# Performance work log

Hardware: AMD Instinct MI355X
Metric: run time of the kernel (lower is better)

## Reference

```python
import jax, jax.numpy as jnp
import numpy as np

D_MODEL = 768
N_HEAD = 12
D_HEAD = D_MODEL // N_HEAD
B, T = 2, 2048


def setup_inputs() -> dict:
    key = jax.random.key(0)
    k1, k2, k3 = jax.random.split(key, 3)
    x = jax.random.normal(k1, (B, T, D_MODEL), dtype=jnp.float32)
    w_attn = jax.random.normal(k2, (D_MODEL, 3 * D_MODEL), dtype=jnp.float32) * (1.0 / np.sqrt(D_MODEL))
    b_attn = jnp.zeros((3 * D_MODEL,), dtype=jnp.float32)
    w_proj = jax.random.normal(k3, (D_MODEL, D_MODEL), dtype=jnp.float32) * (1.0 / np.sqrt(D_MODEL))
    b_proj = jnp.zeros((D_MODEL,), dtype=jnp.float32)
    return {"x": x, "w_attn": w_attn, "b_attn": b_attn, "w_proj": w_proj, "b_proj": b_proj}


def reference(x, w_attn, b_attn, w_proj, b_proj):
    Bq, Tq, C = x.shape
    qkv = x @ w_attn + b_attn                                  # [B, T, 3C]
    qkv = qkv.reshape(Bq, Tq, 3, N_HEAD, D_HEAD)
    q, k, v = qkv[:, :, 0], qkv[:, :, 1], qkv[:, :, 2]         # [B, T, H, Dh]
    scale = 1.0 / np.sqrt(D_HEAD)
    att = jnp.einsum('bqhd,bkhd->bhqk', q, k) * scale          # [B, H, T, T]
    causal = jnp.tril(jnp.ones((Tq, Tq), dtype=bool))
    att = jnp.where(causal[None, None], att, -jnp.inf)
    att = jax.nn.softmax(att, axis=-1)
    y = jnp.einsum('bhqk,bkhd->bqhd', att, v).reshape(Bq, Tq, C)
    return y @ w_proj + b_proj
```

## Files before the change

kernel.cpp:

```cpp
#include <hip/hip_runtime.h>
#include <hip/hip_bf16.h>

#define D_MODEL 768
#define N_HEADS 12
#define D_HEADK 64
#define BB 2
#define TT 2048
#define M_TOK (BB*TT)
#define N_QKV (3*D_MODEL)

using f32x4  = __attribute__((ext_vector_type(4))) float;
using f32x16 = __attribute__((ext_vector_type(16))) float;
using s16x8  = __attribute__((ext_vector_type(8))) short;

__device__ __forceinline__ float fast_exp2(float x) {
    return __builtin_amdgcn_exp2f(x);
}

__device__ __forceinline__ unsigned short f2bf(float f) {
    union { float f; unsigned u; } v; v.f = f;
    unsigned r = v.u + 0x7FFFu + ((v.u >> 16) & 1u);
    return (unsigned short)(r >> 16);
}

__device__ __forceinline__ unsigned cvtpk_bf16(float lo, float hi) {
    unsigned d;
    asm("v_cvt_pk_bf16_f32 %0, %1, %2" : "=v"(d) : "v"(lo), "v"(hi));
    return d;
}

__global__ void xbf_kernel(const float* __restrict__ X, unsigned short* __restrict__ Xb) {
    int idx = (blockIdx.x * 256 + threadIdx.x) * 8;
    float4 v0 = *(const float4*)&X[idx];
    float4 v1 = *(const float4*)&X[idx + 4];
    ushort4 u0, u1;
    u0.x = f2bf(v0.x); u0.y = f2bf(v0.y); u0.z = f2bf(v0.z); u0.w = f2bf(v0.w);
    u1.x = f2bf(v1.x); u1.y = f2bf(v1.y); u1.z = f2bf(v1.z); u1.w = f2bf(v1.w);
    *(ushort4*)&Xb[idx]     = u0;
    *(ushort4*)&Xb[idx + 4] = u1;
}

__global__ void wtrans_kernel(const float* __restrict__ Wa, const float* __restrict__ Wp,
                              unsigned short* __restrict__ Wta, unsigned short* __restrict__ Wtp) {
    const float* W; unsigned short* Wt; int N;
    if (blockIdx.z == 0) { W = Wa; Wt = Wta; N = N_QKV; }
    else                 { W = Wp; Wt = Wtp; N = D_MODEL; }
    int bx = blockIdx.x * 32;
    if (bx >= N) return;
    int by = blockIdx.y * 32;
    __shared__ float tile[32][33];
    int tx = threadIdx.x & 31;
    int ty = threadIdx.x >> 5;
    #pragma unroll
    for (int i = ty; i < 32; i += 8)
        tile[i][tx] = W[(size_t)(by + i) * N + bx + tx];
    __syncthreads();
    #pragma unroll
    for (int i = ty; i < 32; i += 8)
        Wt[(size_t)(bx + i) * D_MODEL + by + tx] = f2bf(tile[tx][i]);
}

__launch_bounds__(256)
__global__ void qkv_kernel(const unsigned short* __restrict__ Xb, const unsigned short* __restrict__ Wt,
                           const float* __restrict__ bias,
                           unsigned short* __restrict__ Qw, unsigned short* __restrict__ Kw,
                           unsigned short* __restrict__ Vw) {
    __shared__ unsigned short As[128][40];
    __shared__ unsigned short Bs[128][40];
    const int m0 = blockIdx.y * 128;
    const int n0 = blockIdx.x * 128;
    const int tid = threadIdx.x;
    const int l  = tid & 63;
    const int w  = tid >> 6;
    const int wr = w >> 1, wc = w & 1;
    const int lr = l & 15, lk = (l >> 4) * 8, li = (l >> 4) * 4;

    f32x4 acc[4][4] = {};
    for (int kt = 0; kt < D_MODEL; kt += 32) {
        #pragma unroll
        for (int p = 0; p < 2; ++p) {
            int ch = tid * 2 + p;
            int r = ch >> 2;
            int c = (ch & 3) * 8;
            *(int4*)&As[r][c] = *(const int4*)&Xb[(size_t)(m0 + r) * D_MODEL + kt + c];
            *(int4*)&Bs[r][c] = *(const int4*)&Wt[(size_t)(n0 + r) * D_MODEL + kt + c];
        }
        __syncthreads();
        s16x8 a[4], bf[4];
        #pragma unroll
        for (int mi = 0; mi < 4; ++mi)
            a[mi] = *(const s16x8*)&As[wr*64 + mi*16 + lr][lk];
        #pragma unroll
        for (int ni = 0; ni < 4; ++ni)
            bf[ni] = *(const s16x8*)&Bs[wc*64 + ni*16 + lr][lk];
        #pragma unroll
        for (int mi = 0; mi < 4; ++mi)
            #pragma unroll
            for (int ni = 0; ni < 4; ++ni)
                acc[mi][ni] = __builtin_amdgcn_mfma_f32_16x16x32_bf16(a[mi], bf[ni], acc[mi][ni], 0, 0, 0);
        __syncthreads();
    }
    #pragma unroll
    for (int ni = 0; ni < 4; ++ni) {
        int ng = n0 + wc*64 + ni*16 + lr;
        int mat = ng / D_MODEL;
        int hd  = ng % D_MODEL;
        int h = hd >> 6, d = hd & 63;
        float bv = bias[ng];
        #pragma unroll
        for (int mi = 0; mi < 4; ++mi) {
            #pragma unroll
            for (int i = 0; i < 4; ++i) {
                int t  = m0 + wr*64 + mi*16 + li + i;
                int b  = t >> 11, tq = t & 2047;
                float val = acc[mi][ni][i] + bv;
                size_t off = ((size_t)(b*N_HEADS + h)*TT + tq)*64 + d;
                if (mat == 0)      Qw[off] = f2bf(val * 0.18033688f);
                else if (mat == 1) Kw[off] = f2bf(val);
                else               Vw[off] = f2bf(val);
            }
        }
    }
}

__launch_bounds__(256)
__global__ void vtrans_kernel(const unsigned short* __restrict__ Vw, unsigned short* __restrict__ Vt) {
    __shared__ unsigned short tile[64][65];
    const int bh = blockIdx.y;
    const int t0 = blockIdx.x * 64;
    const int tid = threadIdx.x;
    const int srow = tid >> 3;
    const int scol = (tid & 7) * 8;
    const unsigned short* src = Vw + (size_t)bh * TT * 64;
    unsigned short* dst = Vt + (size_t)bh * 64 * TT;
    *(int4*)&tile[srow][scol]    = *(const int4*)&src[(size_t)(t0 + srow) * 64 + scol];
    *(int4*)&tile[srow+32][scol] = *(const int4*)&src[(size_t)(t0 + srow + 32) * 64 + scol];
    __syncthreads();
    s16x8 a0, a1;
    #pragma unroll
    for (int j = 0; j < 8; ++j) {
        a0[j] = (short)tile[scol + j][srow];
        a1[j] = (short)tile[scol + j][srow + 32];
    }
    *(s16x8*)&dst[(size_t)srow * TT + t0 + scol]        = a0;
    *(s16x8*)&dst[(size_t)(srow + 32) * TT + t0 + scol] = a1;
}

__device__ __forceinline__ int swz(int r, int c) { return r*64 + (c ^ ((r & 7) << 3)); }

__launch_bounds__(256)
__global__ void attn_kernel(const unsigned short* __restrict__ Q,
                            const unsigned short* __restrict__ Kk,
                            const unsigned short* __restrict__ Vt,
                            unsigned short* __restrict__ Y) {
    __shared__ unsigned short Ks[64*64];
    __shared__ unsigned short Vs[64*64];
    const int bh = blockIdx.y;
    const int qb = gridDim.x - 1 - blockIdx.x;
    const int q0 = qb * 128;
    const int b = bh / N_HEADS, h = bh % N_HEADS;
    const int tid = threadIdx.x;
    const int l  = tid & 63;
    const int w  = tid >> 6;
    const int lq = l & 31;
    const int hi = l >> 5;
    const int srow = tid >> 3;
    const int scol = (tid & 7) * 8;
    const int qw0 = q0 + w * 32;

    const unsigned short* Qp = Q  + (size_t)bh * TT * 64;
    const unsigned short* Kp = Kk + (size_t)bh * TT * 64;
    const unsigned short* Vp = Vt + (size_t)bh * 64 * TT;

    s16x8 qsel[4];
    {
        const unsigned short* qrow = &Qp[(size_t)(qw0 + lq) * 64];
        #pragma unroll
        for (int t = 0; t < 4; ++t) {
            s16x8 qlo = *(const s16x8*)&qrow[16*t];
            s16x8 qhi = *(const s16x8*)&qrow[16*t + 8];
            qsel[t] = hi ? qhi : qlo;
        }
    }

    float mi = -1e30f, si = 0.f;
    f32x16 o0 = {}, o1 = {};

    const int niter = 2 * (qb + 1);
    int4 kp0 = *(const int4*)&Kp[(size_t)srow * 64 + scol];
    int4 kp1 = *(const int4*)&Kp[(size_t)(srow + 32) * 64 + scol];
    int4 vp0 = *(const int4*)&Vp[(size_t)srow * TT + scol];
    int4 vp1 = *(const int4*)&Vp[(size_t)(srow + 32) * TT + scol];

    for (int it = 0; it < niter; ++it) {
        const int kt = it * 64;
        __syncthreads();
        *(int4*)&Ks[swz(srow,      scol)] = kp0;
        *(int4*)&Ks[swz(srow + 32, scol)] = kp1;
        *(int4*)&Vs[swz(srow,      scol)] = vp0;
        *(int4*)&Vs[swz(srow + 32, scol)] = vp1;
        __syncthreads();
        if (it + 1 < niter) {
            const int k2 = kt + 64;
            kp0 = *(const int4*)&Kp[(size_t)(k2 + srow) * 64 + scol];
            kp1 = *(const int4*)&Kp[(size_t)(k2 + srow + 32) * 64 + scol];
            vp0 = *(const int4*)&Vp[(size_t)srow * TT + k2 + scol];
            vp1 = *(const int4*)&Vp[(size_t)(srow + 32) * TT + k2 + scol];
        }
        #pragma unroll
        for (int kti = 0; kti < 2; ++kti) {
            const int kk = kt + kti * 32;
            if (kk > qw0) continue;
            const bool diag = (kk == qw0);
            f32x16 s = {};
            #pragma unroll
            for (int t = 0; t < 4; ++t) {
                s16x8 a = *(const s16x8*)&Ks[swz(kti*32 + lq, 16*t + 8*hi)];
                s = __builtin_amdgcn_mfma_f32_32x32x16_bf16(a, qsel[t], s, 0, 0, 0);
            }
            if (diag) {
                #pragma unroll
                for (int r = 0; r < 16; ++r) {
                    const int kloc = (r & 3) + 8*(r >> 2) + 4*hi;
                    if (kloc > lq) s[r] = -1e30f;
                }
            }
            float lm = s[0];
            #pragma unroll
            for (int r = 1; r < 16; ++r) lm = fmaxf(lm, s[r]);
            if (!__all(lm <= mi + 11.5f)) {
                float pm = fmaxf(lm, __shfl_xor(lm, 32));
                float mn = fmaxf(mi, pm);
                float sf = fast_exp2(mi - mn);
                si *= sf;
                #pragma unroll
                for (int r = 0; r < 16; ++r) {
                    const int qloc = (r & 3) + 8*(r >> 2) + 4*hi;
                    float sfq = __shfl(sf, qloc);
                    o0[r] *= sfq; o1[r] *= sfq;
                }
                mi = mn;
            }
            float e[16];
            float psum = 0.f;
            #pragma unroll
            for (int r = 0; r < 16; ++r) {
                e[r] = fast_exp2(s[r] - mi);
                psum += e[r];
            }
            si += psum;
            #pragma unroll
            for (int s2 = 0; s2 < 2; ++s2) {
                unsigned c0 = cvtpk_bf16(e[8*s2 + 0], e[8*s2 + 1]);
                unsigned c1 = cvtpk_bf16(e[8*s2 + 2], e[8*s2 + 3]);
                unsigned c2 = cvtpk_bf16(e[8*s2 + 4], e[8*s2 + 5]);
                unsigned c3 = cvtpk_bf16(e[8*s2 + 6], e[8*s2 + 7]);
                asm("v_permlane32_swap_b32 %0, %1" : "+v"(c0), "+v"(c2));
                asm("v_permlane32_swap_b32 %0, %1" : "+v"(c1), "+v"(c3));
                union { unsigned u[4]; s16x8 v; } pa;
                pa.u[0] = c0; pa.u[1] = c1; pa.u[2] = c2; pa.u[3] = c3;
                const int kc = kti*32 + 16*s2 + 8*hi;
                s16x8 vb0 = *(const s16x8*)&Vs[swz(lq,      kc)];
                s16x8 vb1 = *(const s16x8*)&Vs[swz(32 + lq, kc)];
                o0 = __builtin_amdgcn_mfma_f32_32x32x16_bf16(pa.v, vb0, o0, 0, 0, 0);
                o1 = __builtin_amdgcn_mfma_f32_32x32x16_bf16(pa.v, vb1, o1, 0, 0, 0);
            }
        }
    }
    float sfull = si + __shfl_xor(si, 32);
    float invf = 1.f / sfull;
    #pragma unroll
    for (int r = 0; r < 16; ++r) {
        const int qloc = (r & 3) + 8*(r >> 2) + 4*hi;
        float iv = __shfl(invf, qloc);
        size_t row = (size_t)(b*TT + qw0 + qloc) * D_MODEL + h*64;
        Y[row + lq]      = f2bf(o0[r] * iv);
        Y[row + 32 + lq] = f2bf(o1[r] * iv);
    }
}

__launch_bounds__(256)
__global__ void proj_kernel(const unsigned short* __restrict__ Y, const unsigned short* __restrict__ Wt,
                            const float* __restrict__ bias, float* __restrict__ Out) {
    __shared__ unsigned short As[128][40];
    __shared__ unsigned short Bs[128][40];
    const int m0 = blockIdx.y * 128;
    const int n0 = blockIdx.x * 128;
    const int tid = threadIdx.x;
    const int l  = tid & 63;
    const int w  = tid >> 6;
    const int wr = w >> 1, wc = w & 1;
    const int lr = l & 15, lk = (l >> 4) * 8, li = (l >> 4) * 4;

    f32x4 acc[4][4] = {};
    for (int kt = 0; kt < D_MODEL; kt += 32) {
        #pragma unroll
        for (int p = 0; p < 2; ++p) {
            int ch = tid * 2 + p;
            int r = ch >> 2;
            int c = (ch & 3) * 8;
            *(int4*)&As[r][c] = *(const int4*)&Y[(size_t)(m0 + r) * D_MODEL + kt + c];
            *(int4*)&Bs[r][c] = *(const int4*)&Wt[(size_t)(n0 + r) * D_MODEL + kt + c];
        }
        __syncthreads();
        s16x8 a[4], bf[4];
        #pragma unroll
        for (int mi = 0; mi < 4; ++mi)
            a[mi] = *(const s16x8*)&As[wr*64 + mi*16 + lr][lk];
        #pragma unroll
        for (int ni = 0; ni < 4; ++ni)
            bf[ni] = *(const s16x8*)&Bs[wc*64 + ni*16 + lr][lk];
        #pragma unroll
        for (int mi = 0; mi < 4; ++mi)
            #pragma unroll
            for (int ni = 0; ni < 4; ++ni)
                acc[mi][ni] = __builtin_amdgcn_mfma_f32_16x16x32_bf16(a[mi], bf[ni], acc[mi][ni], 0, 0, 0);
        __syncthreads();
    }
    #pragma unroll
    for (int ni = 0; ni < 4; ++ni) {
        int ng = n0 + wc*64 + ni*16 + lr;
        float bv = bias[ng];
        #pragma unroll
        for (int mj = 0; mj < 4; ++mj)
            #pragma unroll
            for (int i = 0; i < 4; ++i) {
                int t = m0 + wr*64 + mj*16 + li + i;
                Out[(size_t)t*D_MODEL + ng] = acc[mj][ni][i] + bv;
            }
    }
}

extern "C" void kernel_launch(void* const* d_in, const int* in_sizes, int n_in,
                              void* d_out, int out_size, void* d_ws, size_t ws_size,
                              hipStream_t stream) {
    const float* x      = (const float*)d_in[0];
    const float* w_attn = (const float*)d_in[1];
    const float* b_attn = (const float*)d_in[2];
    const float* w_proj = (const float*)d_in[3];
    const float* b_proj = (const float*)d_in[4];
    float* out = (float*)d_out;

    unsigned short* wt_attn = (unsigned short*)d_ws;
    unsigned short* wt_proj = wt_attn + (size_t)N_QKV * D_MODEL;
    unsigned short* Qw      = wt_proj + (size_t)D_MODEL * D_MODEL;
    unsigned short* Kw      = Qw + (size_t)M_TOK * D_MODEL;
    unsigned short* Vw      = Kw + (size_t)M_TOK * D_MODEL;
    unsigned short* Yw      = Vw + (size_t)M_TOK * D_MODEL;
    unsigned short* Xb      = Yw + (size_t)M_TOK * D_MODEL;
    unsigned short* Vtw     = Xb;

    hipLaunchKernelGGL(xbf_kernel, dim3(M_TOK*D_MODEL/2048), dim3(256), 0, stream, x, Xb);
    hipLaunchKernelGGL(wtrans_kernel, dim3(N_QKV/32, D_MODEL/32, 2), dim3(256), 0, stream,
                       w_attn, w_proj, wt_attn, wt_proj);
    hipLaunchKernelGGL(qkv_kernel, dim3(N_QKV/128, M_TOK/128), dim3(256), 0, stream,
                       Xb, wt_attn, b_attn, Qw, Kw, Vw);
    hipLaunchKernelGGL(vtrans_kernel, dim3(TT/64, BB*N_HEADS), dim3(256), 0, stream,
                       Vw, Vtw);
    hipLaunchKernelGGL(attn_kernel, dim3(TT/128, BB*N_HEADS), dim3(256), 0, stream,
                       Qw, Kw, Vtw, Yw);
    hipLaunchKernelGGL(proj_kernel, dim3(D_MODEL/128, M_TOK/128), dim3(256), 0, stream,
                       Yw, wt_proj, b_proj, out);
}
```

Baseline: 200.5 us.

## Use single-wave attention blocks reading K/V directly from global memory

Restructures the attention kernel so each block is one 64-lane wave handling 32 query rows, with a 4x larger grid. The LDS staging of K and V tiles and the block barriers are removed; K fragments are software-prefetched into registers and V fragments are loaded straight from global memory each iteration. This drops synchronisation and LDS traffic and improves causal load balance. In exchange, K/V are no longer shared across four waves, so global/L2 read traffic rises roughly fourfold and the loads are uncoalesced row-strided reads.

```diff
diff --git a/kernel.cpp b/kernel.cpp
--- a/kernel.cpp
+++ b/kernel.cpp
@@ -146,27 +146,18 @@
     *(s16x8*)&dst[(size_t)(srow + 32) * TT + t0 + scol] = a1;
 }
 
-__device__ __forceinline__ int swz(int r, int c) { return r*64 + (c ^ ((r & 7) << 3)); }
-
-__launch_bounds__(256)
+__launch_bounds__(64)
 __global__ void attn_kernel(const unsigned short* __restrict__ Q,
                             const unsigned short* __restrict__ Kk,
                             const unsigned short* __restrict__ Vt,
                             unsigned short* __restrict__ Y) {
-    __shared__ unsigned short Ks[64*64];
-    __shared__ unsigned short Vs[64*64];
     const int bh = blockIdx.y;
-    const int qb = gridDim.x - 1 - blockIdx.x;
-    const int q0 = qb * 128;
+    const int qci = gridDim.x - 1 - blockIdx.x;
+    const int q0 = qci * 32;
     const int b = bh / N_HEADS, h = bh % N_HEADS;
-    const int tid = threadIdx.x;
-    const int l  = tid & 63;
-    const int w  = tid >> 6;
+    const int l = threadIdx.x;
     const int lq = l & 31;
     const int hi = l >> 5;
-    const int srow = tid >> 3;
-    const int scol = (tid & 7) * 8;
-    const int qw0 = q0 + w * 32;
 
     const unsigned short* Qp = Q  + (size_t)bh * TT * 64;
     const unsigned short* Kp = Kk + (size_t)bh * TT * 64;
@@ -174,7 +165,7 @@
 
     s16x8 qsel[4];
     {
-        const unsigned short* qrow = &Qp[(size_t)(qw0 + lq) * 64];
+        const unsigned short* qrow = &Qp[(size_t)(q0 + lq) * 64];
         #pragma unroll
         for (int t = 0; t < 4; ++t) {
             s16x8 qlo = *(const s16x8*)&qrow[16*t];
@@ -186,85 +177,91 @@
     float mi = -1e30f, si = 0.f;
     f32x16 o0 = {}, o1 = {};
 
-    const int niter = 2 * (qb + 1);
-    int4 kp0 = *(const int4*)&Kp[(size_t)srow * 64 + scol];
-    int4 kp1 = *(const int4*)&Kp[(size_t)(srow + 32) * 64 + scol];
-    int4 vp0 = *(const int4*)&Vp[(size_t)srow * TT + scol];
-    int4 vp1 = *(const int4*)&Vp[(size_t)(srow + 32) * TT + scol];
-
-    for (int it = 0; it < niter; ++it) {
-        const int kt = it * 64;
-        __syncthreads();
-        *(int4*)&Ks[swz(srow,      scol)] = kp0;
-        *(int4*)&Ks[swz(srow + 32, scol)] = kp1;
-        *(int4*)&Vs[swz(srow,      scol)] = vp0;
-        *(int4*)&Vs[swz(srow + 32, scol)] = vp1;
-        __syncthreads();
-        if (it + 1 < niter) {
-            const int k2 = kt + 64;
-            kp0 = *(const int4*)&Kp[(size_t)(k2 + srow) * 64 + scol];
-            kp1 = *(const int4*)&Kp[(size_t)(k2 + srow + 32) * 64 + scol];
-            vp0 = *(const int4*)&Vp[(size_t)srow * TT + k2 + scol];
-            vp1 = *(const int4*)&Vp[(size_t)(srow + 32) * TT + k2 + scol];
-        }
-        #pragma unroll
-        for (int kti = 0; kti < 2; ++kti) {
-            const int kk = kt + kti * 32;
-            if (kk > qw0) continue;
-            const bool diag = (kk == qw0);
-            f32x16 s = {};
-            #pragma unroll
-            for (int t = 0; t < 4; ++t) {
-                s16x8 a = *(const s16x8*)&Ks[swz(kti*32 + lq, 16*t + 8*hi)];
-                s = __builtin_amdgcn_mfma_f32_32x32x16_bf16(a, qsel[t], s, 0, 0, 0);
+    s16x8 ka0 = *(const s16x8*)&Kp[(size_t)lq * 64 + 8*hi];
+    s16x8 ka1 = *(const s16x8*)&Kp[(size_t)lq * 64 + 16 + 8*hi];
+    s16x8 ka2 = *(const s16x8*)&Kp[(size_t)lq * 64 + 32 + 8*hi];
+    s16x8 ka3 = *(const s16x8*)&Kp[(size_t)lq * 64 + 48 + 8*hi];
+
+    for (int kk = 0; kk <= q0; kk += 32) {
+        const int kc = kk + 8*hi;
+        s16x8 vb00 = *(const s16x8*)&Vp[(size_t)lq * TT + kc];
+        s16x8 vb01 = *(const s16x8*)&Vp[(size_t)(32 + lq) * TT + kc];
+        s16x8 vb10 = *(const s16x8*)&Vp[(size_t)lq * TT + kc + 16];
+        s16x8 vb11 = *(const s16x8*)&Vp[(size_t)(32 + lq) * TT + kc + 16];
+
+        f32x16 s = {};
+        s = __builtin_amdgcn_mfma_f32_32x32x16_bf16(ka0, qsel[0], s, 0, 0, 0);
+        s = __builtin_amdgcn_mfma_f32_32x32x16_bf16(ka1, qsel[1], s, 0, 0, 0);
+        s = __builtin_amdgcn_mfma_f32_32x32x16_bf16(ka2, qsel[2], s, 0, 0, 0);
+        s = __builtin_amdgcn_mfma_f32_32x32x16_bf16(ka3, qsel[3], s, 0, 0, 0);
+
+        if (kk + 32 <= q0) {
+            const unsigned short* krow = &Kp[(size_t)(kk + 32 + lq) * 64 + 8*hi];
+            ka0 = *(const s16x8*)&krow[0];
+            ka1 = *(const s16x8*)&krow[16];
+            ka2 = *(const s16x8*)&krow[32];
+            ka3 = *(const s16x8*)&krow[48];
+        }
+
+        if (kk == q0) {
+            #pragma unroll
+            for (int r = 0; r < 16; ++r) {
+                const int kloc = (r & 3) + 8*(r >> 2) + 4*hi;
+                if (kloc > lq) s[r] = -1e30f;
             }
-            if (diag) {
-                #pragma unroll
-                for (int r = 0; r < 16; ++r) {
-                    const int kloc = (r & 3) + 8*(r >> 2) + 4*hi;
-                    if (kloc > lq) s[r] = -1e30f;
-                }
+        }
+
+        float m0a = fmaxf(s[0], s[1]),  m1a = fmaxf(s[2], s[3]);
+        float m2a = fmaxf(s[4], s[5]),  m3a = fmaxf(s[6], s[7]);
+        float m4a = fmaxf(s[8], s[9]),  m5a = fmaxf(s[10], s[11]);
+        float m6a = fmaxf(s[12], s[13]), m7a = fmaxf(s[14], s[15]);
+        float lm = fmaxf(fmaxf(fmaxf(m0a, m1a), fmaxf(m2a, m3a)),
+                         fmaxf(fmaxf(m4a, m5a), fmaxf(m6a, m7a)));
+        if (!__all(lm <= mi + 11.5f)) {
+            float pm = fmaxf(lm, __shfl_xor(lm, 32));
+            float mn = fmaxf(mi, pm);
+            float sf = fast_exp2(mi - mn);
+            si *= sf;
+            #pragma unroll
+            for (int r = 0; r < 16; ++r) {
+                const int qloc = (r & 3) + 8*(r >> 2) + 4*hi;
+                float sfq = __shfl(sf, qloc);
+                o0[r] *= sfq; o1[r] *= sfq;
             }
-            float lm = s[0];
-            #pragma unroll
-            for (int r = 1; r < 16; ++r) lm = fmaxf(lm, s[r]);
-            if (!__all(lm <= mi + 11.5f)) {
-                float pm = fmaxf(lm, __shfl_xor(lm, 32));
-                float mn = fmaxf(mi, pm);
-                float sf = fast_exp2(mi - mn);
-                si *= sf;
-                #pragma unroll
-                for (int r = 0; r < 16; ++r) {
-                    const int qloc = (r & 3) + 8*(r >> 2) + 4*hi;
-                    float sfq = __shfl(sf, qloc);
-                    o0[r] *= sfq; o1[r] *= sfq;
-                }
-                mi = mn;
-            }
-            float e[16];
-            float psum = 0.f;
-            #pragma unroll
-            for (int r = 0; r < 16; ++r) {
-                e[r] = fast_exp2(s[r] - mi);
-                psum += e[r];
-            }
-            si += psum;
-            #pragma unroll
-            for (int s2 = 0; s2 < 2; ++s2) {
-                unsigned c0 = cvtpk_bf16(e[8*s2 + 0], e[8*s2 + 1]);
-                unsigned c1 = cvtpk_bf16(e[8*s2 + 2], e[8*s2 + 3]);
-                unsigned c2 = cvtpk_bf16(e[8*s2 + 4], e[8*s2 + 5]);
-                unsigned c3 = cvtpk_bf16(e[8*s2 + 6], e[8*s2 + 7]);
-                asm("v_permlane32_swap_b32 %0, %1" : "+v"(c0), "+v"(c2));
-                asm("v_permlane32_swap_b32 %0, %1" : "+v"(c1), "+v"(c3));
-                union { unsigned u[4]; s16x8 v; } pa;
-                pa.u[0] = c0; pa.u[1] = c1; pa.u[2] = c2; pa.u[3] = c3;
-                const int kc = kti*32 + 16*s2 + 8*hi;
-                s16x8 vb0 = *(const s16x8*)&Vs[swz(lq,      kc)];
-                s16x8 vb1 = *(const s16x8*)&Vs[swz(32 + lq, kc)];
-                o0 = __builtin_amdgcn_mfma_f32_32x32x16_bf16(pa.v, vb0, o0, 0, 0, 0);
-                o1 = __builtin_amdgcn_mfma_f32_32x32x16_bf16(pa.v, vb1, o1, 0, 0, 0);
-            }
+            mi = mn;
+        }
+        float e[16];
+        #pragma unroll
+        for (int r = 0; r < 16; ++r) e[r] = fast_exp2(s[r] - mi);
+        float p0 = (e[0] + e[1]) + (e[2] + e[3]);
+        float p1 = (e[4] + e[5]) + (e[6] + e[7]);
+        float p2 = (e[8] + e[9]) + (e[10] + e[11]);
+        float p3 = (e[12] + e[13]) + (e[14] + e[15]);
+        si += (p0 + p1) + (p2 + p3);
+
+        {
+            unsigned c0 = cvtpk_bf16(e[0], e[1]);
+            unsigned c1 = cvtpk_bf16(e[2], e[3]);
+            unsigned c2 = cvtpk_bf16(e[4], e[5]);
+            unsigned c3 = cvtpk_bf16(e[6], e[7]);
+            asm("v_permlane32_swap_b32 %0, %1" : "+v"(c0), "+v"(c2));
+            asm("v_permlane32_swap_b32 %0, %1" : "+v"(c1), "+v"(c3));
+            union { unsigned u[4]; s16x8 v; } pa;
+            pa.u[0] = c0; pa.u[1] = c1; pa.u[2] = c2; pa.u[3] = c3;
+            o0 = __builtin_amdgcn_mfma_f32_32x32x16_bf16(pa.v, vb00, o0, 0, 0, 0);
+            o1 = __builtin_amdgcn_mfma_f32_32x32x16_bf16(pa.v, vb01, o1, 0, 0, 0);
+        }
+        {
+            unsigned c0 = cvtpk_bf16(e[8], e[9]);
+            unsigned c1 = cvtpk_bf16(e[10], e[11]);
+            unsigned c2 = cvtpk_bf16(e[12], e[13]);
+            unsigned c3 = cvtpk_bf16(e[14], e[15]);
+            asm("v_permlane32_swap_b32 %0, %1" : "+v"(c0), "+v"(c2));
+            asm("v_permlane32_swap_b32 %0, %1" : "+v"(c1), "+v"(c3));
+            union { unsigned u[4]; s16x8 v; } pa;
+            pa.u[0] = c0; pa.u[1] = c1; pa.u[2] = c2; pa.u[3] = c3;
+            o0 = __builtin_amdgcn_mfma_f32_32x32x16_bf16(pa.v, vb10, o0, 0, 0, 0);
+            o1 = __builtin_amdgcn_mfma_f32_32x32x16_bf16(pa.v, vb11, o1, 0, 0, 0);
         }
     }
     float sfull = si + __shfl_xor(si, 32);
@@ -273,7 +270,7 @@
     for (int r = 0; r < 16; ++r) {
         const int qloc = (r & 3) + 8*(r >> 2) + 4*hi;
         float iv = __shfl(invf, qloc);
-        size_t row = (size_t)(b*TT + qw0 + qloc) * D_MODEL + h*64;
+        size_t row = (size_t)(b*TT + q0 + qloc) * D_MODEL + h*64;
         Y[row + lq]      = f2bf(o0[r] * iv);
         Y[row + 32 + lq] = f2bf(o1[r] * iv);
     }
@@ -357,7 +354,7 @@
                        Xb, wt_attn, b_attn, Qw, Kw, Vw);
     hipLaunchKernelGGL(vtrans_kernel, dim3(TT/64, BB*N_HEADS), dim3(256), 0, stream,
                        Vw, Vtw);
-    hipLaunchKernelGGL(attn_kernel, dim3(TT/128, BB*N_HEADS), dim3(256), 0, stream,
+    hipLaunchKernelGGL(attn_kernel, dim3(TT/32, BB*N_HEADS), dim3(64), 0, stream,
                        Qw, Kw, Vtw, Yw);
     hipLaunchKernelGGL(proj_kernel, dim3(D_MODEL/128, M_TOK/128), dim3(256), 0, stream,
                        Yw, wt_proj, b_proj, out);
```

Result: slower. 231.1 us (+15.3%).

## Split causal attention KV range into two segments and merge partial results

Applied to the files above, without the earlier changes.

Each 128-row query block of the attention kernel now runs as two workgroups. Each covers half of the causal key tiles and writes an unnormalized bf16 partial output plus its running max and sum. A new merge kernel rescales and combines the two partials into the final normalized output. This doubles the grid to even out the triangular causal work across compute units, at the cost of an extra kernel launch, extra global traffic for the partials and statistics, and an additional bf16 rounding of the unnormalized outputs.

```diff
diff --git a/kernel.cpp b/kernel.cpp
--- a/kernel.cpp
+++ b/kernel.cpp
@@ -8,6 +8,7 @@
 #define TT 2048
 #define M_TOK (BB*TT)
 #define N_QKV (3*D_MODEL)
+#define MS_SEG (BB*N_HEADS*TT)
 
 using f32x4  = __attribute__((ext_vector_type(4))) float;
 using f32x16 = __attribute__((ext_vector_type(16))) float;
@@ -21,6 +22,10 @@
     union { float f; unsigned u; } v; v.f = f;
     unsigned r = v.u + 0x7FFFu + ((v.u >> 16) & 1u);
     return (unsigned short)(r >> 16);
+}
+
+__device__ __forceinline__ float bf2f(unsigned short u) {
+    union { unsigned u; float f; } v; v.u = ((unsigned)u) << 16; return v.f;
 }
 
 __device__ __forceinline__ unsigned cvtpk_bf16(float lo, float hi) {
@@ -152,12 +157,16 @@
 __global__ void attn_kernel(const unsigned short* __restrict__ Q,
                             const unsigned short* __restrict__ Kk,
                             const unsigned short* __restrict__ Vt,
-                            unsigned short* __restrict__ Y) {
+                            unsigned short* __restrict__ oA,
+                            unsigned short* __restrict__ oB,
+                            float* __restrict__ ms) {
     __shared__ unsigned short Ks[64*64];
     __shared__ unsigned short Vs[64*64];
     const int bh = blockIdx.y;
-    const int qb = gridDim.x - 1 - blockIdx.x;
-    const int q0 = qb * 128;
+    const int px = blockIdx.x;
+    const int qci = 15 - (px >> 1);
+    const int seg = px & 1;
+    const int q0 = qci * 128;
     const int b = bh / N_HEADS, h = bh % N_HEADS;
     const int tid = threadIdx.x;
     const int l  = tid & 63;
@@ -172,6 +181,11 @@
     const unsigned short* Kp = Kk + (size_t)bh * TT * 64;
     const unsigned short* Vp = Vt + (size_t)bh * 64 * TT;
 
+    const int ntiles  = 2 * (qci + 1);
+    const int n0      = ntiles >> 1;
+    const int t_begin = seg ? n0 : 0;
+    const int t_end   = seg ? ntiles : n0;
+
     s16x8 qsel[4];
     {
         const unsigned short* qrow = &Qp[(size_t)(qw0 + lq) * 64];
@@ -186,13 +200,13 @@
     float mi = -1e30f, si = 0.f;
     f32x16 o0 = {}, o1 = {};
 
-    const int niter = 2 * (qb + 1);
-    int4 kp0 = *(const int4*)&Kp[(size_t)srow * 64 + scol];
-    int4 kp1 = *(const int4*)&Kp[(size_t)(srow + 32) * 64 + scol];
-    int4 vp0 = *(const int4*)&Vp[(size_t)srow * TT + scol];
-    int4 vp1 = *(const int4*)&Vp[(size_t)(srow + 32) * TT + scol];
-
-    for (int it = 0; it < niter; ++it) {
+    const int kb0 = t_begin * 64;
+    int4 kp0 = *(const int4*)&Kp[(size_t)(kb0 + srow) * 64 + scol];
+    int4 kp1 = *(const int4*)&Kp[(size_t)(kb0 + srow + 32) * 64 + scol];
+    int4 vp0 = *(const int4*)&Vp[(size_t)srow * TT + kb0 + scol];
+    int4 vp1 = *(const int4*)&Vp[(size_t)(srow + 32) * TT + kb0 + scol];
+
+    for (int it = t_begin; it < t_end; ++it) {
         const int kt = it * 64;
         __syncthreads();
         *(int4*)&Ks[swz(srow,      scol)] = kp0;
@@ -200,7 +214,7 @@
         *(int4*)&Vs[swz(srow,      scol)] = vp0;
         *(int4*)&Vs[swz(srow + 32, scol)] = vp1;
         __syncthreads();
-        if (it + 1 < niter) {
+        if (it + 1 < t_end) {
             const int k2 = kt + 64;
             kp0 = *(const int4*)&Kp[(size_t)(k2 + srow) * 64 + scol];
             kp1 = *(const int4*)&Kp[(size_t)(k2 + srow + 32) * 64 + scol];
@@ -268,15 +282,47 @@
         }
     }
     float sfull = si + __shfl_xor(si, 32);
-    float invf = 1.f / sfull;
+    if (hi == 0) {
+        const int row = bh * TT + qw0 + lq;
+        ms[seg*MS_SEG + row]            = mi;
+        ms[2*MS_SEG + seg*MS_SEG + row] = sfull;
+    }
+    unsigned short* op = seg ? oB : oA;
     #pragma unroll
     for (int r = 0; r < 16; ++r) {
         const int qloc = (r & 3) + 8*(r >> 2) + 4*hi;
-        float iv = __shfl(invf, qloc);
         size_t row = (size_t)(b*TT + qw0 + qloc) * D_MODEL + h*64;
-        Y[row + lq]      = f2bf(o0[r] * iv);
-        Y[row + 32 + lq] = f2bf(o1[r] * iv);
-    }
+        op[row + lq]      = f2bf(o0[r]);
+        op[row + 32 + lq] = f2bf(o1[r]);
+    }
+}
+
+__launch_bounds__(256)
+__global__ void merge_kernel(const unsigned short* __restrict__ oA,
+                             const unsigned short* __restrict__ oB,
+                             const float* __restrict__ ms,
+                             unsigned short* __restrict__ Yw) {
+    const int gid = blockIdx.x * 256 + threadIdx.x;
+    const int e = gid * 8;
+    const int t = e / D_MODEL;
+    const int c = e % D_MODEL;
+    const int b = t >> 11, q = t & 2047;
+    const int h = c >> 6;
+    const int row = (b * N_HEADS + h) * TT + q;
+    float m0 = ms[row],            m1 = ms[MS_SEG + row];
+    float s0 = ms[2*MS_SEG + row], s1 = ms[3*MS_SEG + row];
+    float m  = fmaxf(m0, m1);
+    float a0 = fast_exp2(m0 - m), a1 = fast_exp2(m1 - m);
+    float inv = 1.f / (s0 * a0 + s1 * a1);
+    float w0 = a0 * inv, w1 = a1 * inv;
+    s16x8 va = *(const s16x8*)&oA[e];
+    s16x8 vb = *(const s16x8*)&oB[e];
+    s16x8 out;
+    #pragma unroll
+    for (int j = 0; j < 8; ++j)
+        out[j] = (short)f2bf(bf2f((unsigned short)va[j]) * w0 +
+                             bf2f((unsigned short)vb[j]) * w1);
+    *(s16x8*)&Yw[e] = out;
 }
 
 __launch_bounds__(256)
@@ -349,6 +395,9 @@
     unsigned short* Yw      = Vw + (size_t)M_TOK * D_MODEL;
     unsigned short* Xb      = Yw + (size_t)M_TOK * D_MODEL;
     unsigned short* Vtw     = Xb;
+    unsigned short* oA      = Vw;
+    unsigned short* oB      = Yw;
+    float*          msbuf   = (float*)d_ws;
 
     hipLaunchKernelGGL(xbf_kernel, dim3(M_TOK*D_MODEL/2048), dim3(256), 0, stream, x, Xb);
     hipLaunchKernelGGL(wtrans_kernel, dim3(N_QKV/32, D_MODEL/32, 2), dim3(256), 0, stream,
@@ -357,8 +406,10 @@
                        Xb, wt_attn, b_attn, Qw, Kw, Vw);
     hipLaunchKernelGGL(vtrans_kernel, dim3(TT/64, BB*N_HEADS), dim3(256), 0, stream,
                        Vw, Vtw);
-    hipLaunchKernelGGL(attn_kernel, dim3(TT/128, BB*N_HEADS), dim3(256), 0, stream,
-                       Qw, Kw, Vtw, Yw);
+    hipLaunchKernelGGL(attn_kernel, dim3(32, BB*N_HEADS), dim3(256), 0, stream,
+                       Qw, Kw, Vtw, oA, oB, msbuf);
+    hipLaunchKernelGGL(merge_kernel, dim3(M_TOK*D_MODEL/8/256), dim3(256), 0, stream,
+                       oA, oB, msbuf, Yw);
     hipLaunchKernelGGL(proj_kernel, dim3(D_MODEL/128, M_TOK/128), dim3(256), 0, stream,
                        Yw, wt_proj, b_proj, out);
 }
```

Measured after the change: 195.2 us. -2.6%, faster.
